# Performance work log

Hardware: AMD Instinct MI355X
Metric: run time of the kernel (lower is better)

## Reference

```python
import jax, jax.numpy as jnp
import numpy as np

NUM_CLASSES = 10  # CINIC-10


def setup_inputs() -> dict:
    key = jax.random.key(0)
    k1, k2 = jax.random.split(key)
    embeddings = jax.random.normal(k1, (131072, 512), dtype=jnp.float32)
    labels = jax.random.randint(k2, (131072,), 0, NUM_CLASSES)
    return {"embeddings": embeddings, "labels": labels}


def reference(embeddings, labels):
    # Per-class mean (prototypes) as a segment reduction. With all classes
    # present, torch.unique(labels) == [0..9] sorted, so the remapped
    # target_indices equal labels directly.
    n = embeddings.shape[0]
    sums = jax.ops.segment_sum(embeddings, labels, num_segments=NUM_CLASSES)  # [C, d]
    counts = jax.ops.segment_sum(jnp.ones((n,), embeddings.dtype), labels,
                                 num_segments=NUM_CLASSES)                    # [C]
    prototypes = sums / counts[:, None]

    # Squared Euclidean distances: ||e||^2 + ||p||^2 - 2 e.p  (== cdist(...)**2)
    sq_e = jnp.sum(embeddings * embeddings, axis=1, keepdims=True)  # [B, 1]
    sq_p = jnp.sum(prototypes * prototypes, axis=1)                 # [C]
    d2 = sq_e + sq_p[None, :] - 2.0 * (embeddings @ prototypes.T)   # [B, C]
    d2 = jnp.maximum(d2, 0.0)

    logits = -d2
    logp = jax.nn.log_softmax(logits, axis=-1)
    loss = -jnp.mean(jnp.take_along_axis(logp, labels[:, None], axis=1))
    return (loss, logits)
```

## Files before the change

kernel.cpp:

```cpp
#include <hip/hip_runtime.h>

#define NROWS   131072
#define DIMS    512
#define NC      10
#define SEG_BLOCKS 1024
#define SUMSTRIDE 5120

typedef __attribute__((ext_vector_type(8))) short short8;
typedef __attribute__((ext_vector_type(4))) float floatx4;


static __device__ __forceinline__ unsigned int pk2(float lo, float hi) {
    return (__float_as_uint(hi) & 0xFFFF0000u) | (__float_as_uint(lo) >> 16);
}

static __device__ __forceinline__ short8 pack8(const float4 a, const float4 b) {
    union { unsigned int u[4]; short8 v; } r;
    r.u[0] = pk2(a.x, a.y);
    r.u[1] = pk2(a.z, a.w);
    r.u[2] = pk2(b.x, b.y);
    r.u[3] = pk2(b.z, b.w);
    return r.v;
}


__global__ __launch_bounds__(256) void k_seg(const float* __restrict__ E,
                                             const int* __restrict__ L,
                                             float* __restrict__ part,
                                             int* __restrict__ counts) {
    __shared__ float4 R[NC * 128];
    __shared__ int lc[16];
    const int tid  = threadIdx.x;
    const int half = tid >> 7;
    const int dt   = tid & 127;
    if (tid < 16) lc[tid] = 0;
    __syncthreads();

    const int rows0 = blockIdx.x * 128;
    const float4* Ev = (const float4*)E;

    float4 z = {0.f, 0.f, 0.f, 0.f};
    float4 a0=z,a1=z,a2=z,a3=z,a4=z,a5=z,a6=z,a7=z,a8=z,a9=z;

    int idx = (rows0 + half) * 128 + dt;
    float4 v0 = Ev[idx];
    float4 v1 = Ev[idx + 256];
    int l0 = L[rows0 + half];
    int l1 = L[rows0 + 2 + half];

    for (int i = 0; i < 64; ++i) {
        float4 v2; int l2;
        const bool pf = (i < 62);
        if (pf) {
            v2 = Ev[idx + 512];
            l2 = L[rows0 + 2 * i + 4 + half];
        }
        if (dt == 0) atomicAdd(&lc[l0], 1);
        switch (l0) {
            case 0: a0.x+=v0.x; a0.y+=v0.y; a0.z+=v0.z; a0.w+=v0.w; break;
            case 1: a1.x+=v0.x; a1.y+=v0.y; a1.z+=v0.z; a1.w+=v0.w; break;
            case 2: a2.x+=v0.x; a2.y+=v0.y; a2.z+=v0.z; a2.w+=v0.w; break;
            case 3: a3.x+=v0.x; a3.y+=v0.y; a3.z+=v0.z; a3.w+=v0.w; break;
            case 4: a4.x+=v0.x; a4.y+=v0.y; a4.z+=v0.z; a4.w+=v0.w; break;
            case 5: a5.x+=v0.x; a5.y+=v0.y; a5.z+=v0.z; a5.w+=v0.w; break;
            case 6: a6.x+=v0.x; a6.y+=v0.y; a6.z+=v0.z; a6.w+=v0.w; break;
            case 7: a7.x+=v0.x; a7.y+=v0.y; a7.z+=v0.z; a7.w+=v0.w; break;
            case 8: a8.x+=v0.x; a8.y+=v0.y; a8.z+=v0.z; a8.w+=v0.w; break;
            default: a9.x+=v0.x; a9.y+=v0.y; a9.z+=v0.z; a9.w+=v0.w; break;
        }
        v0 = v1; l0 = l1;
        if (pf) { v1 = v2; l1 = l2; }
        idx += 256;
    }

    if (half) {
        R[0*128+dt]=a0; R[1*128+dt]=a1; R[2*128+dt]=a2; R[3*128+dt]=a3;
        R[4*128+dt]=a4; R[5*128+dt]=a5; R[6*128+dt]=a6; R[7*128+dt]=a7;
        R[8*128+dt]=a8; R[9*128+dt]=a9;
    }
    __syncthreads();
    if (!half) {
        float4* dst = (float4*)(part + (size_t)blockIdx.x * SUMSTRIDE);
        float4 t;
#define MERGE_ST(c, ac)                                                       \
        t = R[(c)*128 + dt];                                                  \
        t.x += ac.x; t.y += ac.y; t.z += ac.z; t.w += ac.w;                   \
        dst[(c)*128 + dt] = t;
        MERGE_ST(0,a0) MERGE_ST(1,a1) MERGE_ST(2,a2) MERGE_ST(3,a3)
        MERGE_ST(4,a4) MERGE_ST(5,a5) MERGE_ST(6,a6) MERGE_ST(7,a7)
        MERGE_ST(8,a8) MERGE_ST(9,a9)
#undef MERGE_ST
    }
    if (tid < 16) counts[blockIdx.x * 16 + tid] = lc[tid];
}


__global__ __launch_bounds__(256) void k_red(const float* __restrict__ part,
                                             float* __restrict__ psum8) {
    __shared__ float m[128];
    const int t   = threadIdx.x;
    const int col = t & 127, kh = t >> 7;
    const int cc  = blockIdx.x % 40;
    const int kc  = blockIdx.x / 40;
    const int e   = cc * 128 + col;

    const float* base = part + (size_t)(kc * 128 + kh * 64) * SUMSTRIDE + e;
    float s0=0.f, s1=0.f, s2=0.f, s3=0.f;
    for (int j = 0; j < 64; j += 4) {
        s0 += base[(size_t)(j + 0) * SUMSTRIDE];
        s1 += base[(size_t)(j + 1) * SUMSTRIDE];
        s2 += base[(size_t)(j + 2) * SUMSTRIDE];
        s3 += base[(size_t)(j + 3) * SUMSTRIDE];
    }
    float s = (s0 + s1) + (s2 + s3);
    if (kh) m[col] = s;
    __syncthreads();
    if (!kh) psum8[kc * SUMSTRIDE + e] = s + m[col];
}


__global__ __launch_bounds__(512) void k_pp(const float* __restrict__ psum8,
                                            const int* __restrict__ counts,
                                            float* __restrict__ p2,
                                            float* __restrict__ pn,
                                            float* __restrict__ out) {
    __shared__ float P[16 * DIMS];
    __shared__ int tmp[512];
    __shared__ int cnt[16];
    const int t = threadIdx.x;

    {
        const int c0 = t & 15, chunk = t >> 4;
        int s = 0;
        for (int j = 0; j < 32; ++j) s += counts[(chunk * 32 + j) * 16 + c0];
        tmp[t] = s;
    }
    __syncthreads();
    if (t < 16) {
        int n = 0;
        for (int ch = 0; ch < 32; ++ch) n += tmp[ch * 16 + t];
        cnt[t] = n;
    }
    if (t == 0) out[0] = 0.f;
    __syncthreads();

    for (int e = t; e < 16 * DIMS; e += 512) {
        const int c = e >> 9;
        float val = 0.f;
        if (c < NC) {
            float s = 0.f;
#pragma unroll
            for (int j = 0; j < 8; ++j) s += psum8[j * SUMSTRIDE + e];
            val = 2.f * s / (float)cnt[c];
        }
        p2[e] = val;
        P[e] = val;
    }
    __syncthreads();

    const int w = t >> 6, lane = t & 63;
    const float4* Pv = (const float4*)P;
    for (int sdx = 0; sdx < 2; ++sdx) {
        const int c = w + sdx * 8;
        float4 a = Pv[c * 128 + lane * 2];
        float4 b = Pv[c * 128 + lane * 2 + 1];
        float ss = a.x*a.x + a.y*a.y + a.z*a.z + a.w*a.w
                 + b.x*b.x + b.y*b.y + b.z*b.z + b.w*b.w;
        ss += __shfl_xor(ss, 1);  ss += __shfl_xor(ss, 2);
        ss += __shfl_xor(ss, 4);  ss += __shfl_xor(ss, 8);
        ss += __shfl_xor(ss, 16); ss += __shfl_xor(ss, 32);
        if (lane == 0) pn[c] = 0.25f * ss;
    }
}


__global__ __launch_bounds__(256, 2) void k_main(const float* __restrict__ E,
                                                 const int* __restrict__ L,
                                                 const float* __restrict__ p2,
                                                 const float* __restrict__ pn,
                                                 float* __restrict__ out) {
    const int tid  = threadIdx.x;
    const int wid  = tid >> 6, lane = tid & 63;
    const int c16  = lane & 15, quad = lane >> 4;

    short8 bf[16];
    const float4* P = (const float4*)p2;
#pragma unroll
    for (int kt = 0; kt < 16; ++kt) {
        float4 a = P[c16 * 128 + kt * 8 + quad * 2];
        float4 b = P[c16 * 128 + kt * 8 + quad * 2 + 1];
        bf[kt] = pack8(a, b);
    }
    const float pnc = pn[c16];

    float lossp = 0.f;
    const int gw = blockIdx.x * 4 + wid;
    for (int t = gw; t < 8192; t += 4096) {
        const int tile  = 8191 - t;
        const int rbase = tile * 16;
        const float4* A = (const float4*)(E + (size_t)(rbase + c16) * DIMS);

        floatx4 acc = {0.f, 0.f, 0.f, 0.f};
        float nrm = 0.f;
#pragma unroll
        for (int kt = 0; kt < 16; ++kt) {
            float4 a = A[kt * 8 + quad * 2];
            float4 b = A[kt * 8 + quad * 2 + 1];
            nrm += a.x*a.x + a.y*a.y + a.z*a.z + a.w*a.w;
            nrm += b.x*b.x + b.y*b.y + b.z*b.z + b.w*b.w;
            acc = __builtin_amdgcn_mfma_f32_16x16x32_bf16(pack8(a, b), bf[kt],
                                                          acc, 0, 0, 0);
        }
        nrm += __shfl_xor(nrm, 16);
        nrm += __shfl_xor(nrm, 32);

#pragma unroll
        for (int i = 0; i < 4; ++i) {
            const int row = rbase + quad * 4 + i;
            const float nr = __shfl(nrm, quad * 4 + i);
            float lg = acc[i] - nr - pnc;
            lg = fminf(lg, 0.f);
            float ml = (c16 < NC) ? lg : -3.0e38f;
            ml = fmaxf(ml, __shfl_xor(ml, 1));
            ml = fmaxf(ml, __shfl_xor(ml, 2));
            ml = fmaxf(ml, __shfl_xor(ml, 4));
            ml = fmaxf(ml, __shfl_xor(ml, 8));
            float ex = (c16 < NC) ? __expf(lg - ml) : 0.f;
            ex += __shfl_xor(ex, 1);
            ex += __shfl_xor(ex, 2);
            ex += __shfl_xor(ex, 4);
            ex += __shfl_xor(ex, 8);
            const float lse = ml + __logf(ex);
            if (c16 < NC) out[1 + row * NC + c16] = lg;
            const int lab = L[row];
            if (c16 == lab) lossp += lse - lg;
        }
    }

    lossp += __shfl_xor(lossp, 1);  lossp += __shfl_xor(lossp, 2);
    lossp += __shfl_xor(lossp, 4);  lossp += __shfl_xor(lossp, 8);
    lossp += __shfl_xor(lossp, 16); lossp += __shfl_xor(lossp, 32);
    __shared__ float ls[4];
    if (lane == 0) ls[wid] = lossp;
    __syncthreads();
    if (tid == 0)
        atomicAdd(out, (ls[0] + ls[1] + ls[2] + ls[3]) * (1.0f / (float)NROWS));
}


extern "C" void kernel_launch(void* const* d_in, const int* in_sizes, int n_in,
                              void* d_out, int out_size, void* d_ws, size_t ws_size,
                              hipStream_t stream) {
    const float* E = (const float*)d_in[0];
    const int*   L = (const int*)d_in[1];
    float* out = (float*)d_out;
    char* ws = (char*)d_ws;

    float* part   = (float*)ws;
    float* psum8  = (float*)(ws + 20971520);
    int*   counts = (int*)  (ws + 21135360);
    float* p2     = (float*)(ws + 21200896);
    float* pn     = (float*)(ws + 21233664);

    k_seg <<<SEG_BLOCKS, 256, 0, stream>>>(E, L, part, counts);
    k_red <<<320,        256, 0, stream>>>(part, psum8);
    k_pp  <<<1,          512, 0, stream>>>(psum8, counts, p2, pn, out);
    k_main<<<1024,       256, 0, stream>>>(E, L, p2, pn, out);
}
```

Baseline: 453.4 us.

## Emit bf16 embedding copy and row norms in segment pass for main kernel

The segment-sum kernel, which already streams all embeddings, now also writes a truncated bf16 copy of each row and its squared norm to workspace. The main distance kernel reads the half-size bf16 copy and the precomputed norms instead of re-reading fp32 embeddings and recomputing norms. This halves the main kernel's embedding read traffic. In exchange, the first pass gains a 128 MB write plus a per-iteration wave-wide shuffle reduction, and the workspace must be large enough to hold the copy.

```diff
diff --git a/kernel.cpp b/kernel.cpp
--- a/kernel.cpp
+++ b/kernel.cpp
@@ -27,12 +27,17 @@
 __global__ __launch_bounds__(256) void k_seg(const float* __restrict__ E,
                                              const int* __restrict__ L,
                                              float* __restrict__ part,
-                                             int* __restrict__ counts) {
+                                             int* __restrict__ counts,
+                                             uint2* __restrict__ E16,
+                                             float* __restrict__ norms) {
     __shared__ float4 R[NC * 128];
+    __shared__ float ns[4 * 64];
     __shared__ int lc[16];
     const int tid  = threadIdx.x;
     const int half = tid >> 7;
     const int dt   = tid & 127;
+    const int wid  = tid >> 6;
+    const int lane = tid & 63;
     if (tid < 16) lc[tid] = 0;
     __syncthreads();
 
@@ -56,6 +61,18 @@
             l2 = L[rows0 + 2 * i + 4 + half];
         }
         if (dt == 0) atomicAdd(&lc[l0], 1);
+
+        uint2 uu;
+        uu.x = pk2(v0.x, v0.y);
+        uu.y = pk2(v0.z, v0.w);
+        E16[idx] = uu;
+
+        float p = v0.x*v0.x + v0.y*v0.y + v0.z*v0.z + v0.w*v0.w;
+        p += __shfl_xor(p, 1);  p += __shfl_xor(p, 2);
+        p += __shfl_xor(p, 4);  p += __shfl_xor(p, 8);
+        p += __shfl_xor(p, 16); p += __shfl_xor(p, 32);
+        if (lane == 0) ns[wid * 64 + i] = p;
+
         switch (l0) {
             case 0: a0.x+=v0.x; a0.y+=v0.y; a0.z+=v0.z; a0.w+=v0.w; break;
             case 1: a1.x+=v0.x; a1.y+=v0.y; a1.z+=v0.z; a1.w+=v0.w; break;
@@ -90,6 +107,10 @@
         MERGE_ST(4,a4) MERGE_ST(5,a5) MERGE_ST(6,a6) MERGE_ST(7,a7)
         MERGE_ST(8,a8) MERGE_ST(9,a9)
 #undef MERGE_ST
+    }
+    if (tid < 128) {
+        const int i2 = tid >> 1, h2 = tid & 1;
+        norms[rows0 + tid] = ns[(2*h2)*64 + i2] + ns[(2*h2+1)*64 + i2];
     }
     if (tid < 16) counts[blockIdx.x * 16 + tid] = lc[tid];
 }
@@ -174,7 +195,8 @@
 }
 
 
-__global__ __launch_bounds__(256, 2) void k_main(const float* __restrict__ E,
+__global__ __launch_bounds__(256, 2) void k_main(const ushort* __restrict__ E16,
+                                                 const float* __restrict__ norms,
                                                  const int* __restrict__ L,
                                                  const float* __restrict__ p2,
                                                  const float* __restrict__ pn,
@@ -198,26 +220,20 @@
     for (int t = gw; t < 8192; t += 4096) {
         const int tile  = 8191 - t;
         const int rbase = tile * 16;
-        const float4* A = (const float4*)(E + (size_t)(rbase + c16) * DIMS);
+        const short8* A = (const short8*)(E16 + (size_t)(rbase + c16) * DIMS);
+        const float nmine = norms[rbase + c16];
 
         floatx4 acc = {0.f, 0.f, 0.f, 0.f};
-        float nrm = 0.f;
 #pragma unroll
         for (int kt = 0; kt < 16; ++kt) {
-            float4 a = A[kt * 8 + quad * 2];
-            float4 b = A[kt * 8 + quad * 2 + 1];
-            nrm += a.x*a.x + a.y*a.y + a.z*a.z + a.w*a.w;
-            nrm += b.x*b.x + b.y*b.y + b.z*b.z + b.w*b.w;
-            acc = __builtin_amdgcn_mfma_f32_16x16x32_bf16(pack8(a, b), bf[kt],
-                                                          acc, 0, 0, 0);
-        }
-        nrm += __shfl_xor(nrm, 16);
-        nrm += __shfl_xor(nrm, 32);
+            acc = __builtin_amdgcn_mfma_f32_16x16x32_bf16(A[kt * 4 + quad],
+                                                          bf[kt], acc, 0, 0, 0);
+        }
 
 #pragma unroll
         for (int i = 0; i < 4; ++i) {
             const int row = rbase + quad * 4 + i;
-            const float nr = __shfl(nrm, quad * 4 + i);
+            const float nr = __shfl(nmine, quad * 4 + i);
             float lg = acc[i] - nr - pnc;
             lg = fminf(lg, 0.f);
             float ml = (c16 < NC) ? lg : -3.0e38f;
@@ -261,9 +277,11 @@
     int*   counts = (int*)  (ws + 21135360);
     float* p2     = (float*)(ws + 21200896);
     float* pn     = (float*)(ws + 21233664);
-
-    k_seg <<<SEG_BLOCKS, 256, 0, stream>>>(E, L, part, counts);
+    float* norms  = (float*)(ws + 21233728);
+    uint2* E16    = (uint2*)(ws + 21758016);
+
+    k_seg <<<SEG_BLOCKS, 256, 0, stream>>>(E, L, part, counts, E16, norms);
     k_red <<<320,        256, 0, stream>>>(part, psum8);
     k_pp  <<<1,          512, 0, stream>>>(psum8, counts, p2, pn, out);
-    k_main<<<1024,       256, 0, stream>>>(E, L, p2, pn, out);
-}
+    k_main<<<1024,       256, 0, stream>>>((const ushort*)E16, norms, L, p2, pn, out);
+}
```

After: 453.1 us. About the same (-0.1%).
